# Performance work log

Measured on AMD Instinct MI355X. Metric: run time of the kernel, lower is better.

The kernel has to match this reference:

```python
import jax, jax.numpy as jnp
import numpy as np

EPS = 1e-5


def setup_inputs() -> dict:
    key = jax.random.key(0)
    ks = jax.random.split(key, 8)
    N, M, D = 8192, 8192, 512
    s = 1.0 / np.sqrt(D)
    return {
        "x": jax.random.normal(ks[0], (N, D), jnp.float32),
        "x_hat": jax.random.normal(ks[1], (1, M, D), jnp.float32),
        "Wq": jax.random.normal(ks[2], (D, D), jnp.float32) * s,
        "bq": jnp.zeros((D,), jnp.float32),
        "Wk": jax.random.normal(ks[3], (D, D), jnp.float32) * s,
        "bk": jnp.zeros((D,), jnp.float32),
        "Wv": jax.random.normal(ks[4], (D, D), jnp.float32) * s,
        "bv": jnp.zeros((D,), jnp.float32),
        "Wout": jax.random.normal(ks[5], (D, 2 * D), jnp.float32) * s,
        "bout": jnp.zeros((D,), jnp.float32),
        "gamma": jnp.ones((D,), jnp.float32),
        "beta": jnp.zeros((D,), jnp.float32),
    }


def reference(x, x_hat, Wq, bq, Wk, bk, Wv, bv, Wout, bout, gamma, beta):
    D = x.shape[-1]
    # LayerNorm over last dim
    mu = jnp.mean(x, axis=-1, keepdims=True)
    var = jnp.mean(jnp.square(x - mu), axis=-1, keepdims=True)
    xn = (x - mu) * jax.lax.rsqrt(var + EPS) * gamma + beta
    xr = xn.reshape(1, -1, D)                                   # [1, N, D]
    q = jnp.einsum('bnd,ed->bne', xr, Wq) + bq                  # [1, N, E]
    k = jnp.einsum('bmd,ed->bme', x_hat, Wk) + bk               # [1, M, E]
    qk = jnp.einsum('bne,bme->bnm', q, k) / jnp.sqrt(jnp.float32(D))
    score = jax.nn.softmax(qk, axis=-1)                         # [1, N, M]
    attn = jnp.einsum('bnm,bme->bne', score, k)                 # K used as values
    out_v = jnp.einsum('bne,fe->bnf', attn, Wv) + bv            # v-proj AFTER attention
    cat = jnp.concatenate([q, out_v], axis=-1)                  # [1, N, 2E]
    out = jnp.einsum('bnc,dc->bnd', cat, Wout) + bout           # [1, N, D]
    return out + xr
```

## Files before the change

### kernel.cpp

```cpp
#include <hip/hip_runtime.h>

typedef __attribute__((ext_vector_type(8))) short short8;
typedef __attribute__((ext_vector_type(4))) short short4v;
typedef __attribute__((ext_vector_type(4))) float f32x4;
typedef __attribute__((ext_vector_type(2))) float f32x2;
typedef __attribute__((ext_vector_type(2))) unsigned uint2v;

#define MFMA(a,b,c) __builtin_amdgcn_mfma_f32_16x16x32_bf16((a),(b),(c),0,0,0)

__device__ __forceinline__ short f2b(float f) {
  unsigned u = __builtin_bit_cast(unsigned, f);
  unsigned r = (u + 0x7fffu + ((u >> 16) & 1u)) >> 16;
  return (short)r;
}
__device__ __forceinline__ float b2f(short h) {
  unsigned u = ((unsigned)(unsigned short)h) << 16;
  return __builtin_bit_cast(float, u);
}
__device__ __forceinline__ unsigned pack2(float a, float b) {
  return (unsigned)(unsigned short)f2b(a) | ((unsigned)(unsigned short)f2b(b) << 16);
}

__device__ __forceinline__ float wred(float v) {
  #pragma unroll
  for (int m = 32; m; m >>= 1) v += __shfl_xor(v, m, 64);
  return v;
}

__device__ __forceinline__ void glds16(const short* g, short* l) {
  __builtin_amdgcn_global_load_lds(
      (const __attribute__((address_space(1))) unsigned*)g,
      (__attribute__((address_space(3))) unsigned*)l, 16, 0, 0);
}

__global__ __launch_bounds__(256) void cvt_kernel(const float* __restrict__ src,
                                                  short* __restrict__ dst, int n4) {
  int i = blockIdx.x * 256 + threadIdx.x;
  if (i < n4) {
    f32x4 v = *(const f32x4*)(src + (size_t)i * 4);
    short4v o = { f2b(v[0]), f2b(v[1]), f2b(v[2]), f2b(v[3]) };
    *(short4v*)(dst + (size_t)i * 4) = o;
  }
}

__global__ __launch_bounds__(256) void tcvt_kernel(const float* __restrict__ src,
                                                   short* __restrict__ dst) {
  __shared__ float tile[32][33];
  int bx = blockIdx.x & 15, by = blockIdx.x >> 4;
  int tx = threadIdx.x & 31, ty = threadIdx.x >> 5;
  #pragma unroll
  for (int i = 0; i < 4; ++i)
    tile[ty + 8 * i][tx] = src[(size_t)(by * 32 + ty + 8 * i) * 512 + bx * 32 + tx];
  __syncthreads();
  #pragma unroll
  for (int i = 0; i < 4; ++i)
    dst[(size_t)(bx * 32 + ty + 8 * i) * 512 + by * 32 + tx] = f2b(tile[tx][ty + 8 * i]);
}

__global__ __launch_bounds__(256) void bsf_kernel(const float* __restrict__ Wout,
                                                  const float* __restrict__ bvv,
                                                  const float* __restrict__ bout,
                                                  float* __restrict__ biasf,
                                                  float* __restrict__ zb) {
  int d = blockIdx.x, tid = threadIdx.x;
  int wid = tid >> 6, lane = tid & 63;
  __shared__ float red[4];
  float s = Wout[(size_t)d * 1024 + 512 + tid] * bvv[tid]
          + Wout[(size_t)d * 1024 + 768 + tid] * bvv[tid + 256];
  s = wred(s);
  if (!lane) red[wid] = s;
  __syncthreads();
  if (!tid) biasf[d] = bout[d] + red[0] + red[1] + red[2] + red[3];
  if (d == 0) { zb[tid] = 0.f; zb[tid + 256] = 0.f; }
}

__global__ __launch_bounds__(256) void ln_kernel(const float* __restrict__ x,
                                                 const float* __restrict__ gamma,
                                                 const float* __restrict__ beta,
                                                 float* __restrict__ xnf,
                                                 short* __restrict__ xnb) {
  int wid = threadIdx.x >> 6, lane = threadIdx.x & 63;
  int n = blockIdx.x * 4 + wid;
  const float* xp = x + (size_t)n * 512 + lane * 8;
  f32x4 v0 = *(const f32x4*)xp;
  f32x4 v1 = *(const f32x4*)(xp + 4);
  float s = v0[0] + v0[1] + v0[2] + v0[3] + v1[0] + v1[1] + v1[2] + v1[3];
  float mu = wred(s) * (1.f / 512.f);
  f32x4 d0 = v0 - mu, d1 = v1 - mu;
  float q = d0[0]*d0[0] + d0[1]*d0[1] + d0[2]*d0[2] + d0[3]*d0[3]
          + d1[0]*d1[0] + d1[1]*d1[1] + d1[2]*d1[2] + d1[3]*d1[3];
  float var = wred(q) * (1.f / 512.f);
  float rs = rsqrtf(var + 1e-5f);
  int c = lane * 8;
  f32x4 g0 = *(const f32x4*)(gamma + c), g1 = *(const f32x4*)(gamma + c + 4);
  f32x4 b0 = *(const f32x4*)(beta + c),  b1 = *(const f32x4*)(beta + c + 4);
  f32x4 o0 = d0 * rs * g0 + b0;
  f32x4 o1 = d1 * rs * g1 + b1;
  float* op = xnf + (size_t)n * 512 + c;
  *(f32x4*)op = o0;
  *(f32x4*)(op + 4) = o1;
  short8 ob = { f2b(o0[0]), f2b(o0[1]), f2b(o0[2]), f2b(o0[3]),
                f2b(o1[0]), f2b(o1[1]), f2b(o1[2]), f2b(o1[3]) };
  *(short8*)(xnb + (size_t)n * 512 + c) = ob;
}

template<int MODE>
__global__ __launch_bounds__(256, 2) void gemm_nt(
    const short* __restrict__ A, const short* __restrict__ B,
    int K, int lda, int ldb,
    const float* __restrict__ bias,
    short* __restrict__ Cb, int ldc, int coff,
    short* __restrict__ CT, int ldct,
    const float* __restrict__ resid, float* __restrict__ Cf) {
  __shared__ short As[128][72];
  __shared__ short Bs[128][72];
  int tid = threadIdx.x;
  int w = tid >> 6, lane = tid & 63;
  int li = lane & 15, g = lane >> 4;
  int wr = w >> 1, wc = w & 1;
  int bm = blockIdx.x, bn = blockIdx.y;
  f32x4 acc[4][4] = {};
  int nK = K >> 6;
  for (int kk = 0; kk < nK; ++kk) {
    short8 av[4], bv4[4];
    #pragma unroll
    for (int c = 0; c < 4; ++c) {
      int q = c * 256 + tid;
      int r = q >> 3, s = q & 7;
      av[c]  = *(const short8*)(A + (size_t)(bm * 128 + r) * lda + kk * 64 + s * 8);
      bv4[c] = *(const short8*)(B + (size_t)(bn * 128 + r) * ldb + kk * 64 + s * 8);
    }
    __syncthreads();
    #pragma unroll
    for (int c = 0; c < 4; ++c) {
      int q = c * 256 + tid;
      int r = q >> 3, s = q & 7;
      *(short8*)&As[r][s * 8] = av[c];
      *(short8*)&Bs[r][s * 8] = bv4[c];
    }
    __syncthreads();
    #pragma unroll
    for (int kc = 0; kc < 2; ++kc) {
      short8 af[4], bfr[4];
      #pragma unroll
      for (int i = 0; i < 4; ++i)
        af[i] = *(const short8*)&As[wr * 64 + i * 16 + li][kc * 32 + (g << 3)];
      #pragma unroll
      for (int j = 0; j < 4; ++j)
        bfr[j] = *(const short8*)&Bs[wc * 64 + j * 16 + li][kc * 32 + (g << 3)];
      #pragma unroll
      for (int i = 0; i < 4; ++i)
        #pragma unroll
        for (int j = 0; j < 4; ++j)
          acc[i][j] = MFMA(af[i], bfr[j], acc[i][j]);
    }
  }
  int row0 = bm * 128 + wr * 64, col0 = bn * 128 + wc * 64;
  #pragma unroll
  for (int i = 0; i < 4; ++i) {
    #pragma unroll
    for (int j = 0; j < 4; ++j) {
      int col = col0 + j * 16 + li;
      float bcol = bias[col];
      #pragma unroll
      for (int r = 0; r < 4; ++r) {
        int row = row0 + i * 16 + (g << 2) + r;
        float vv = acc[i][j][r] + bcol;
        if (MODE == 2) {
          Cf[(size_t)row * 512 + col] = vv + resid[(size_t)row * 512 + col];
        } else {
          Cb[(size_t)row * ldc + coff + col] = f2b(vv);
        }
      }
    }
  }
  if (MODE == 1) {
    #pragma unroll
    for (int i2 = 0; i2 < 2; ++i2) {
      int base = row0 + i2 * 32;
      #pragma unroll
      for (int j = 0; j < 4; ++j) {
        int col = col0 + j * 16 + li;
        float bcol = bias[col];
        #pragma unroll
        for (int rp = 0; rp < 2; ++rp) {
          int r = rp * 2;
          uint2v pk;
          pk[0] = pack2(acc[i2 * 2][j][r]     + bcol, acc[i2 * 2 + 1][j][r]     + bcol);
          pk[1] = pack2(acc[i2 * 2][j][r + 1] + bcol, acc[i2 * 2 + 1][j][r + 1] + bcol);
          *(uint2v*)&CT[(size_t)col * ldct + base + 8 * g + 2 * r] = pk;
        }
      }
    }
  }
}

#define SCALE 0.044194173824159216f
__global__ __launch_bounds__(512, 2) void attn_kernel(
    const short* __restrict__ Qg,
    const short* __restrict__ Kg,
    const short* __restrict__ KTg,
    short* __restrict__ U,
    float* __restrict__ lp) {
  __shared__ short Kl[2][32][520];
  __shared__ short Pl[2][128][32];
  int tid = threadIdx.x, w = tid >> 6, lane = tid & 63;
  int li = lane & 15, g = lane >> 4;
  int qb = blockIdx.x >> 2, ms = blockIdx.x & 3;
  int key_base = ms * 2048;

  short8 qf[16];
  {
    size_t row = (size_t)qb * 128 + w * 16 + li;
    const short* qp = Qg + row * 1024 + (g << 3);
    #pragma unroll
    for (int c = 0; c < 16; ++c) qf[c] = *(const short8*)(qp + c * 32);
  }
  f32x4 acc[8][4] = {};
  float lac[4] = {0.f, 0.f, 0.f, 0.f};

  #pragma unroll
  for (int c = 0; c < 4; ++c) {
    int r = c * 8 + w;
    glds16(Kg + (size_t)(key_base + r) * 512 + lane * 8, &Kl[0][r][0]);
  }
  __syncthreads();

  for (int t = 0; t < 64; ++t) {
    int cur = t & 1, nxt = cur ^ 1;
    if (t < 63) {
      #pragma unroll
      for (int c = 0; c < 4; ++c) {
        int r = c * 8 + w;
        glds16(Kg + (size_t)(key_base + (t + 1) * 32 + r) * 512 + lane * 8, &Kl[nxt][r][0]);
      }
    }
    short8 b2[4];
    #pragma unroll
    for (int et = 0; et < 4; ++et) {
      int e = (w << 6) + (et << 4) + li;
      b2[et] = *(const short8*)(KTg + (size_t)e * 8192 + key_base + t * 32 + (g << 3));
    }
    f32x4 s0 = {0, 0, 0, 0}, s1 = {0, 0, 0, 0};
    __builtin_amdgcn_s_setprio(1);
    #pragma unroll
    for (int c = 0; c < 16; ++c) {
      short8 k0 = *(const short8*)&Kl[cur][li][c * 32 + (g << 3)];
      short8 k1 = *(const short8*)&Kl[cur][16 + li][c * 32 + (g << 3)];
      s0 = MFMA(qf[c], k0, s0);
      s1 = MFMA(qf[c], k1, s1);
    }
    __builtin_amdgcn_s_setprio(0);
    #pragma unroll
    for (int r = 0; r < 4; ++r) {
      float p0 = __expf(s0[r] * SCALE);
      float p1 = __expf(s1[r] * SCALE);
      lac[r] += p0 + p1;
      int prow = (w << 4) + (g << 2) + r;
      *(unsigned*)&Pl[cur][prow][2 * li] = pack2(p0, p1);
    }
    __syncthreads();
    __builtin_amdgcn_s_setprio(1);
    #pragma unroll
    for (int qt = 0; qt < 8; ++qt) {
      short8 a = *(const short8*)&Pl[cur][qt * 16 + li][g << 3];
      #pragma unroll
      for (int et = 0; et < 4; ++et)
        acc[qt][et] = MFMA(a, b2[et], acc[qt][et]);
    }
    __builtin_amdgcn_s_setprio(0);
  }

  short* Up = U + (((size_t)ms * 8192) + (size_t)qb * 128) * 512;
  #pragma unroll
  for (int qt = 0; qt < 8; ++qt)
    #pragma unroll
    for (int et = 0; et < 4; ++et)
      #pragma unroll
      for (int r = 0; r < 4; ++r) {
        int row = (qt << 4) + (g << 2) + r;
        int col = (w << 6) + (et << 4) + li;
        Up[(size_t)row * 512 + col] = f2b(acc[qt][et][r]);
      }
  #pragma unroll
  for (int r = 0; r < 4; ++r) {
    float v = lac[r];
    v += __shfl_xor(v, 1, 16);
    v += __shfl_xor(v, 2, 16);
    v += __shfl_xor(v, 4, 16);
    v += __shfl_xor(v, 8, 16);
    if (!li) lp[ms * 8192 + qb * 128 + (w << 4) + (g << 2) + r] = v;
  }
}

__global__ __launch_bounds__(256) void combine_kernel(const short* __restrict__ U,
                                                      const float* __restrict__ lp,
                                                      short* __restrict__ cat2) {
  int idx = blockIdx.x * 256 + threadIdx.x;
  int n = idx >> 6, e8 = (idx & 63) << 3;
  float s[8] = {0, 0, 0, 0, 0, 0, 0, 0};
  float li = 0.f;
  #pragma unroll
  for (int msv = 0; msv < 4; ++msv) {
    short8 v = *(const short8*)(U + ((size_t)msv * 8192 + n) * 512 + e8);
    #pragma unroll
    for (int j = 0; j < 8; ++j) s[j] += b2f(v[j]);
    li += lp[msv * 8192 + n];
  }
  float inv = 1.f / li;
  short8 o;
  #pragma unroll
  for (int j = 0; j < 8; ++j) o[j] = f2b(s[j] * inv);
  *(short8*)(cat2 + (size_t)n * 1024 + 512 + e8) = o;
}

extern "C" void kernel_launch(void* const* d_in, const int* in_sizes, int n_in,
                              void* d_out, int out_size, void* d_ws, size_t ws_size,
                              hipStream_t stream) {
  const float* x     = (const float*)d_in[0];
  const float* xhat  = (const float*)d_in[1];
  const float* Wq    = (const float*)d_in[2];
  const float* bq    = (const float*)d_in[3];
  const float* Wk    = (const float*)d_in[4];
  const float* bk    = (const float*)d_in[5];
  const float* Wv    = (const float*)d_in[6];
  const float* bv    = (const float*)d_in[7];
  const float* Wout  = (const float*)d_in[8];
  const float* bout  = (const float*)d_in[9];
  const float* gamma = (const float*)d_in[10];
  const float* beta  = (const float*)d_in[11];
  float* out = (float*)d_out;

  char* ws = (char*)d_ws;
  const size_t MB = 1024 * 1024;
  float* xnf   = (float*)(ws + 0);
  short* cat2  = (short*)(ws + 16 * MB);
  short* kb    = (short*)(ws + 32 * MB);
  short* ktb   = (short*)(ws + 40 * MB);
  short* W12   = (short*)(ws + 48 * MB);
  float* bsf   = (float*)(ws + 49 * MB);
  float* lp    = (float*)(ws + 49 * MB + 65536);
  short* Woutb = (short*)(ws + 50 * MB);
  short* WvTb  = (short*)(ws + 51 * MB);
  float* zb    = (float*)(ws + 51 * MB + 524288);
  short* U     = (short*)(ws + 52 * MB);
  short* xnb   = (short*)(ws + 52 * MB);
  short* xhb   = (short*)(ws + 60 * MB);
  short* Wqb   = (short*)(ws + 68 * MB);
  short* Wkb   = (short*)(ws + 69 * MB);
  (void)ws_size; (void)in_sizes; (void)n_in; (void)out_size;

  cvt_kernel<<<4096, 256, 0, stream>>>(xhat, xhb, 1048576);
  cvt_kernel<<<256, 256, 0, stream>>>(Wq, Wqb, 65536);
  cvt_kernel<<<256, 256, 0, stream>>>(Wk, Wkb, 65536);
  cvt_kernel<<<512, 256, 0, stream>>>(Wout, W12, 131072);
  cvt_kernel<<<512, 256, 0, stream>>>(Wout, Woutb, 131072);
  tcvt_kernel<<<256, 256, 0, stream>>>(Wv, WvTb);
  bsf_kernel<<<512, 256, 0, stream>>>(Wout, bv, bout, bsf, zb);
  gemm_nt<0><<<dim3(4, 4), 256, 0, stream>>>(Woutb + 512, WvTb, 512, 1024, 512, zb,
                                             W12, 1024, 512, nullptr, 0, nullptr, nullptr);
  ln_kernel<<<2048, 256, 0, stream>>>(x, gamma, beta, xnf, xnb);
  gemm_nt<0><<<dim3(64, 4), 256, 0, stream>>>(xnb, Wqb, 512, 512, 512, bq,
                                              cat2, 1024, 0, nullptr, 0, nullptr, nullptr);
  gemm_nt<1><<<dim3(64, 4), 256, 0, stream>>>(xhb, Wkb, 512, 512, 512, bk,
                                              kb, 512, 0, ktb, 8192, nullptr, nullptr);
  attn_kernel<<<256, 512, 0, stream>>>(cat2, kb, ktb, U, lp);
  combine_kernel<<<2048, 256, 0, stream>>>(U, lp, cat2);
  gemm_nt<2><<<dim3(64, 4), 256, 0, stream>>>(cat2, W12, 1024, 1024, 1024, bsf,
                                              nullptr, 0, 0, nullptr, 0, xnf, out);
}
```

Before: 374.1 us.

## Double-buffer GEMM tiles with direct global-to-LDS loads and XOR swizzle

The projection GEMM kernel now stages A/B tiles straight into LDS with async global-to-LDS loads into two buffers, prefetching the next K-slice while the current one is multiplied. The padded layout is replaced by an XOR-swizzled layout to avoid bank conflicts without padding. The s_setprio hints are also removed from the attention kernel. Shared memory per block doubles, which may limit occupancy, and the glds16 swizzle addressing must match the read pattern exactly.

```diff
diff --git a/kernel.cpp b/kernel.cpp
--- a/kernel.cpp
+++ b/kernel.cpp
@@ -112,49 +112,52 @@
     short* __restrict__ Cb, int ldc, int coff,
     short* __restrict__ CT, int ldct,
     const float* __restrict__ resid, float* __restrict__ Cf) {
-  __shared__ short As[128][72];
-  __shared__ short Bs[128][72];
+  __shared__ short As[2][128][64];
+  __shared__ short Bs[2][128][64];
   int tid = threadIdx.x;
   int w = tid >> 6, lane = tid & 63;
   int li = lane & 15, g = lane >> 4;
   int wr = w >> 1, wc = w & 1;
   int bm = blockIdx.x, bn = blockIdx.y;
+  int lrow = lane >> 3;
+  int lchunk = (lane & 7) ^ lrow;
   f32x4 acc[4][4] = {};
   int nK = K >> 6;
+
+  #define STAGE(buf, kk) do {                                                     \
+    _Pragma("unroll")                                                             \
+    for (int i_ = 0; i_ < 4; ++i_) {                                              \
+      int r0_ = (w * 4 + i_) * 8;                                                 \
+      const short* ga_ = A + (size_t)(bm * 128 + r0_ + lrow) * lda + (size_t)(kk) * 64 + lchunk * 8; \
+      const short* gb_ = B + (size_t)(bn * 128 + r0_ + lrow) * ldb + (size_t)(kk) * 64 + lchunk * 8; \
+      glds16(ga_, &As[buf][r0_][0]);                                              \
+      glds16(gb_, &Bs[buf][r0_][0]);                                              \
+    } } while (0)
+
+  STAGE(0, 0);
+  __syncthreads();
   for (int kk = 0; kk < nK; ++kk) {
-    short8 av[4], bv4[4];
-    #pragma unroll
-    for (int c = 0; c < 4; ++c) {
-      int q = c * 256 + tid;
-      int r = q >> 3, s = q & 7;
-      av[c]  = *(const short8*)(A + (size_t)(bm * 128 + r) * lda + kk * 64 + s * 8);
-      bv4[c] = *(const short8*)(B + (size_t)(bn * 128 + r) * ldb + kk * 64 + s * 8);
-    }
-    __syncthreads();
-    #pragma unroll
-    for (int c = 0; c < 4; ++c) {
-      int q = c * 256 + tid;
-      int r = q >> 3, s = q & 7;
-      *(short8*)&As[r][s * 8] = av[c];
-      *(short8*)&Bs[r][s * 8] = bv4[c];
-    }
-    __syncthreads();
+    int cb = kk & 1;
+    if (kk + 1 < nK) STAGE(cb ^ 1, kk + 1);
     #pragma unroll
     for (int kc = 0; kc < 2; ++kc) {
       short8 af[4], bfr[4];
       #pragma unroll
       for (int i = 0; i < 4; ++i)
-        af[i] = *(const short8*)&As[wr * 64 + i * 16 + li][kc * 32 + (g << 3)];
+        af[i] = *(const short8*)&As[cb][wr * 64 + i * 16 + li][(((kc << 2) + g) ^ (li & 7)) << 3];
       #pragma unroll
       for (int j = 0; j < 4; ++j)
-        bfr[j] = *(const short8*)&Bs[wc * 64 + j * 16 + li][kc * 32 + (g << 3)];
+        bfr[j] = *(const short8*)&Bs[cb][wc * 64 + j * 16 + li][(((kc << 2) + g) ^ (li & 7)) << 3];
       #pragma unroll
       for (int i = 0; i < 4; ++i)
         #pragma unroll
         for (int j = 0; j < 4; ++j)
           acc[i][j] = MFMA(af[i], bfr[j], acc[i][j]);
     }
-  }
+    __syncthreads();
+  }
+  #undef STAGE
+
   int row0 = bm * 128 + wr * 64, col0 = bn * 128 + wc * 64;
   #pragma unroll
   for (int i = 0; i < 4; ++i) {
@@ -242,7 +245,6 @@
       b2[et] = *(const short8*)(KTg + (size_t)e * 8192 + key_base + t * 32 + (g << 3));
     }
     f32x4 s0 = {0, 0, 0, 0}, s1 = {0, 0, 0, 0};
-    __builtin_amdgcn_s_setprio(1);
     #pragma unroll
     for (int c = 0; c < 16; ++c) {
       short8 k0 = *(const short8*)&Kl[cur][li][c * 32 + (g << 3)];
@@ -250,7 +252,6 @@
       s0 = MFMA(qf[c], k0, s0);
       s1 = MFMA(qf[c], k1, s1);
     }
-    __builtin_amdgcn_s_setprio(0);
     #pragma unroll
     for (int r = 0; r < 4; ++r) {
       float p0 = __expf(s0[r] * SCALE);
@@ -260,7 +261,6 @@
       *(unsigned*)&Pl[cur][prow][2 * li] = pack2(p0, p1);
     }
     __syncthreads();
-    __builtin_amdgcn_s_setprio(1);
     #pragma unroll
     for (int qt = 0; qt < 8; ++qt) {
       short8 a = *(const short8*)&Pl[cur][qt * 16 + li][g << 3];
@@ -268,7 +268,6 @@
       for (int et = 0; et < 4; ++et)
         acc[qt][et] = MFMA(a, b2[et], acc[qt][et]);
     }
-    __builtin_amdgcn_s_setprio(0);
   }
 
   short* Up = U + (((size_t)ms * 8192) + (size_t)qb * 128) * 512;
```

Measured after the change: 317.0 us. -15.3%, faster.
